# Optimization experiments

Measured on AMD Instinct MI355X. Metric: run time of the kernel, lower is better.

## Reference

```python
import jax, jax.numpy as jnp
import numpy as np

DIM = 2048
NUM_GATES = 8
TOP_N = 2
EPS = 1e-9
B, N = 2, 4096
CAPACITY_FACTOR = 1.25  # train
MIN_EXPERT_CAPACITY = 4
THRESHOLD = np.array([EPS, 0.2], dtype=np.float32)  # [eps, *threshold_train]


def setup_inputs() -> dict:
    key = jax.random.key(0)
    kx, kw, kp = jax.random.split(key, 3)
    x = jax.random.normal(kx, (B, N, DIM), jnp.float32)
    W = jax.random.normal(kw, (NUM_GATES, DIM), jnp.float32) * 0.02  # Linear(dim, num_gates, bias=False)
    probs = jax.random.uniform(kp, (TOP_N, B, N), jnp.float32)       # the uniform draw inside forward
    return {"x": x, "W": W, "probs": probs}


def reference(x, W, probs):
    b, n, d = x.shape
    cap = max(min(n, int(n * CAPACITY_FACTOR / NUM_GATES)), MIN_EXPERT_CAPACITY)
    dt = x.dtype

    gate_logits = jnp.einsum('bnd,ed->bne', x, W)            # [b,n,e]
    raw_gates = jax.nn.softmax(gate_logits, axis=-1)
    gates, gate_idx = jax.lax.top_k(raw_gates, TOP_N)        # [b,n,k]
    gates = jnp.moveaxis(gates, -1, 0)                       # [k,b,n]
    gate_idx = jnp.moveaxis(gate_idx, -1, 0)                 # [k,b,n]
    one_hot_e = jax.nn.one_hot(gate_idx, NUM_GATES, dtype=dt)  # [k,b,n,e]

    denom = jnp.clip(gates.sum(0, keepdims=True), EPS, None)
    gates = gates / denom                                    # renormalized top-n gates

    thr = jnp.clip(jnp.asarray(THRESHOLD, dt), EPS, None)[:, None, None]
    should_route = probs < gates / thr                       # [k,b,n]
    should_route = should_route.at[0].set(True)              # top-1 always routes
    mask = one_hot_e * should_route[..., None].astype(dt)    # [k,b,n,e]

    # exclusive cumsum over the sequence dim (position of each token in its expert queue)
    mask_cumsum = jnp.cumsum(mask, axis=2) - mask            # [k,b,n,e]

    combine = jnp.zeros((b, n, NUM_GATES, cap), dt)
    prev_expert_count = jnp.zeros((b, 1, NUM_GATES), dt)
    final_masks = []
    for k in range(TOP_N):  # tiny fixed loop over top-n slots
        pos = (mask_cumsum[k] + prev_expert_count) * mask[k]          # [b,n,e]
        mk = mask[k] * (pos < float(cap)).astype(dt)                  # drop over-capacity tokens
        prev_expert_count = prev_expert_count + mk.sum(axis=1, keepdims=True)
        pos_flat = pos.sum(axis=-1)                                   # [b,n]
        mflat = mk.sum(axis=-1)                                       # [b,n] in {0,1}
        pos_oh = jax.nn.one_hot(pos_flat.astype(jnp.int32), cap, dtype=dt)  # out-of-range -> zeros (safe_one_hot)
        # gates_k * mask_flat * one_hot_e * pos_one_hot; mflat^2 == mflat, one_hot_e*mflat == mk
        combine = combine + jnp.einsum('bn,bne,bnc->bnec', gates[k] * mflat, mk, pos_oh)
        final_masks.append(mk)

    dispatch = (combine != 0).astype(dt)
    # straight-through dispatch tensor
    dispatch = dispatch + combine - jax.lax.stop_gradient(combine)

    # training losses (mask[0] was mutated in-place in torch -> use final capacity-clipped top-1 mask)
    density_1 = final_masks[0].mean(axis=1)                  # [b,e]
    density_1_proxy = raw_gates.mean(axis=1)                 # [b,e]
    balance_loss = (density_1_proxy * density_1).mean() * float(NUM_GATES ** 2)
    router_z_loss = jnp.mean(jnp.square(jax.nn.logsumexp(gate_logits, axis=-1)))

    return dispatch, combine, balance_loss, router_z_loss
```

## Files before the change

kernel.cpp:

```cpp
#include <hip/hip_runtime.h>


#define DIMX 2048
#define NG   8
#define NB   2
#define NSEQ 4096
#define NTOK (NB*NSEQ)
#define CAPE 640
#define ROW  (NG*CAPE)
#define DCNT ((size_t)NTOK*ROW)

typedef float vfloat4 __attribute__((ext_vector_type(4)));

struct Ws {
  int   pk[NTOK];
  float g0[NTOK];
  float g1[NTOK];
  float z2[NTOK];
  int   pos0[NTOK];
  int   pos1[NTOK];
  float raws[(size_t)NTOK*NG];
  float proxy[16];
  float zpart[16];
  int   cnt0[16];
};

__global__ __launch_bounds__(512) void kgate(const float* __restrict__ x,
                                             const float* __restrict__ W,
                                             const float* __restrict__ probs,
                                             Ws* __restrict__ ws) {
  int tid = threadIdx.x;
  int wave = tid >> 6, lane = tid & 63;
  int token = blockIdx.x * 8 + wave;

  const float4* xp = (const float4*)(x + (size_t)token * DIMX);
  const float4* W4 = (const float4*)W;

  float acc[NG] = {0.f,0.f,0.f,0.f,0.f,0.f,0.f,0.f};
#pragma unroll
  for (int j = 0; j < 8; ++j) {
    float4 xj = xp[j * 64 + lane];
#pragma unroll
    for (int e = 0; e < NG; ++e) {
      float4 w = W4[e * 512 + j * 64 + lane];
      acc[e] = fmaf(xj.x, w.x, acc[e]);
      acc[e] = fmaf(xj.y, w.y, acc[e]);
      acc[e] = fmaf(xj.z, w.z, acc[e]);
      acc[e] = fmaf(xj.w, w.w, acc[e]);
    }
  }
#pragma unroll
  for (int e = 0; e < NG; ++e) {
#pragma unroll
    for (int off = 32; off > 0; off >>= 1) acc[e] += __shfl_xor(acc[e], off, 64);
  }

  float m = acc[0];
#pragma unroll
  for (int e = 1; e < NG; ++e) m = fmaxf(m, acc[e]);
  float ex[NG], s = 0.f;
#pragma unroll
  for (int e = 0; e < NG; ++e) { ex[e] = expf(acc[e] - m); s += ex[e]; }
  float raw[NG];
#pragma unroll
  for (int e = 0; e < NG; ++e) raw[e] = ex[e] / s;

  int e0i = 0; float g0v = raw[0];
#pragma unroll
  for (int e = 1; e < NG; ++e) if (raw[e] > g0v) { g0v = raw[e]; e0i = e; }
  int e1i = -1; float g1v = -1.f;
#pragma unroll
  for (int e = 0; e < NG; ++e) if (e != e0i && raw[e] > g1v) { g1v = raw[e]; e1i = e; }

  float denom = g0v + g1v;
  if (denom < 1e-9f) denom = 1e-9f;
  float g0n = g0v / denom, g1n = g1v / denom;

  float p1 = probs[NTOK + token];
  int rte = (p1 < (g1n / 0.2f)) ? 1 : 0;

  float lse = m + logf(s);

  if (lane < NG) ws->raws[(size_t)token * NG + lane] = raw[lane];
  if (lane == 0) {
    ws->pk[token] = e0i | (e1i << 4) | (rte << 8);
    ws->g0[token] = g0n;  ws->g1[token] = g1n;
    ws->z2[token] = lse * lse;
  }
}

__global__ __launch_bounds__(256) void kscan(Ws* __restrict__ ws) {
  __shared__ int   wtot[4];
  __shared__ float wsum[4];
  __shared__ float zsum[4];
  int be = blockIdx.x, b = be >> 3, e = be & 7;
  int t = threadIdx.x, wave = t >> 6, lane = t & 63;
  int base = b * NSEQ;

  int pk[16];
  {
    const int4* pp = (const int4*)(ws->pk + base + t * 16);
#pragma unroll
    for (int j = 0; j < 4; ++j) {
      int4 v = pp[j];
      pk[4*j] = v.x; pk[4*j+1] = v.y; pk[4*j+2] = v.z; pk[4*j+3] = v.w;
    }
  }

  float ps = 0.f;
#pragma unroll
  for (int i = 0; i < 16; ++i) ps += ws->raws[(size_t)(base + t * 16 + i) * NG + e];
#pragma unroll
  for (int off = 32; off > 0; off >>= 1) ps += __shfl_xor(ps, off, 64);
  if (lane == 0) wsum[wave] = ps;

  float zs = 0.f;
  if (t < 128) {
    float4 v = ((const float4*)ws->z2)[be * 128 + t];
    zs = v.x + v.y + v.z + v.w;
  }
#pragma unroll
  for (int off = 32; off > 0; off >>= 1) zs += __shfl_xor(zs, off, 64);
  if (lane == 0) zsum[wave] = zs;

  int cnt = 0;
#pragma unroll
  for (int i = 0; i < 16; ++i) cnt += ((pk[i] & 15) == e);
  int incl = cnt;
#pragma unroll
  for (int off = 1; off < 64; off <<= 1) { int v = __shfl_up(incl, off, 64); if (lane >= off) incl += v; }
  if (lane == 63) wtot[wave] = incl;
  __syncthreads();
  int woff = 0, tot = 0;
#pragma unroll
  for (int w = 0; w < 4; ++w) { int v = wtot[w]; tot += v; if (w < wave) woff += v; }
  int c0 = min(tot, CAPE);
  int p = woff + incl - cnt;
#pragma unroll
  for (int i = 0; i < 16; ++i) {
    if ((pk[i] & 15) == e) { ws->pos0[base + t * 16 + i] = (p < CAPE) ? p : -1; ++p; }
  }
  __syncthreads();

  cnt = 0;
#pragma unroll
  for (int i = 0; i < 16; ++i) cnt += ((((pk[i] >> 4) & 15) == e) && (pk[i] & 0x100));
  incl = cnt;
#pragma unroll
  for (int off = 1; off < 64; off <<= 1) { int v = __shfl_up(incl, off, 64); if (lane >= off) incl += v; }
  if (lane == 63) wtot[wave] = incl;
  __syncthreads();
  woff = 0;
#pragma unroll
  for (int w = 0; w < 4; ++w) { int v = wtot[w]; if (w < wave) woff += v; }
  p = woff + incl - cnt;
#pragma unroll
  for (int i = 0; i < 16; ++i) {
    if ((((pk[i] >> 4) & 15) == e)) {
      if (pk[i] & 0x100) { int q = p + c0; ws->pos1[base + t * 16 + i] = (q < CAPE) ? q : -1; ++p; }
      else               { ws->pos1[base + t * 16 + i] = -1; }
    }
  }

  if (t == 0) {
    ws->proxy[be] = wsum[0] + wsum[1] + wsum[2] + wsum[3];
    ws->zpart[be] = zsum[0] + zsum[1] + zsum[2] + zsum[3];
    ws->cnt0[be]  = c0;
  }
}

__global__ __launch_bounds__(256) void kout(const Ws* __restrict__ ws, float* __restrict__ out) {
  int t = threadIdx.x;

#pragma unroll
  for (int tk = 0; tk < 2; ++tk) {
    int token = blockIdx.x * 2 + tk;
    int pkv = ws->pk[token];
    int e0 = pkv & 15, e1 = (pkv >> 4) & 15;
    int p0 = ws->pos0[token], p1 = ws->pos1[token];
    float g0 = ws->g0[token], g1 = ws->g1[token];
    int o0 = (p0 >= 0) ? e0 * CAPE + p0 : -16;
    int o1 = (p1 >= 0) ? e1 * CAPE + p1 : -16;

    float* drow = out + (size_t)token * ROW;
    float* crow = out + DCNT + (size_t)token * ROW;

#pragma unroll
    for (int c = 0; c < 5; ++c) {
      int off = c * 1024 + t * 4;
      int r0 = o0 - off, r1 = o1 - off;
      vfloat4 dv, cv;
      dv.x = ((r0 == 0) | (r1 == 0)) ? 1.f : 0.f;
      dv.y = ((r0 == 1) | (r1 == 1)) ? 1.f : 0.f;
      dv.z = ((r0 == 2) | (r1 == 2)) ? 1.f : 0.f;
      dv.w = ((r0 == 3) | (r1 == 3)) ? 1.f : 0.f;
      cv.x = (r0 == 0) ? g0 : ((r1 == 0) ? g1 : 0.f);
      cv.y = (r0 == 1) ? g0 : ((r1 == 1) ? g1 : 0.f);
      cv.z = (r0 == 2) ? g0 : ((r1 == 2) ? g1 : 0.f);
      cv.w = (r0 == 3) ? g0 : ((r1 == 3) ? g1 : 0.f);
      __builtin_nontemporal_store(dv, (vfloat4*)(drow + off));
      __builtin_nontemporal_store(cv, (vfloat4*)(crow + off));
    }
  }

  if (blockIdx.x == 0 && t == 0) {
    float bal = 0.f, z = 0.f;
#pragma unroll
    for (int i = 0; i < 16; ++i) {
      bal += (ws->proxy[i] * (1.f / NSEQ)) * ((float)ws->cnt0[i] * (1.f / NSEQ));
      z   += ws->zpart[i];
    }
    out[2 * DCNT]     = bal * 4.f;
    out[2 * DCNT + 1] = z * (1.f / NTOK);
  }
}

extern "C" void kernel_launch(void* const* d_in, const int* in_sizes, int n_in,
                              void* d_out, int out_size, void* d_ws, size_t ws_size,
                              hipStream_t stream) {
  const float* x     = (const float*)d_in[0];
  const float* W     = (const float*)d_in[1];
  const float* probs = (const float*)d_in[2];
  float* out = (float*)d_out;
  Ws* ws = (Ws*)d_ws;

  kgate<<<NTOK / 8, 512, 0, stream>>>(x, W, probs, ws);
  kscan<<<16, 256, 0, stream>>>(ws);
  kout<<<NTOK / 2, 256, 0, stream>>>(ws, out);
}
```

Baseline: 97.02 us.

## Zero dispatch tensor inside gate kernel and scatter ones in output kernel

The gate kernel gains extra blocks, interleaved with the gating blocks, that write zeros over the whole dispatch tensor. The aim is to overlap that store traffic with the memory-bound gate matmul and its reads of x. The output kernel then writes only the combine tensor densely and sets at most two dispatch entries per token to 1.0 with scalar stores. Total bytes written stay the same, so any gain depends on better overlap and less work in the last kernel, while the extra blocks compete with the gate blocks for bandwidth.

Result: faster. 90.22 us (-7.0%).

```diff
diff --git a/kernel.cpp b/kernel.cpp
--- a/kernel.cpp
+++ b/kernel.cpp
@@ -25,13 +25,37 @@
   int   cnt0[16];
 };
 
-__global__ __launch_bounds__(512) void kgate(const float* __restrict__ x,
-                                             const float* __restrict__ W,
-                                             const float* __restrict__ probs,
-                                             Ws* __restrict__ ws) {
+__global__ __launch_bounds__(512) void kfat(const float* __restrict__ x,
+                                            const float* __restrict__ W,
+                                            const float* __restrict__ probs,
+                                            Ws* __restrict__ ws,
+                                            float* __restrict__ out) {
+  int bid = blockIdx.x;
   int tid = threadIdx.x;
+
+  int g;
+  if (bid < 2048) {
+    g = bid >> 1;
+    if (!(bid & 1)) {
+      vfloat4* o4 = (vfloat4*)out;
+      long base = (long)g * 5120 + tid;
+      vfloat4 z = {0.f, 0.f, 0.f, 0.f};
+#pragma unroll
+      for (int k = 0; k < 10; ++k) __builtin_nontemporal_store(z, o4 + base + k * 512);
+      return;
+    }
+  } else {
+    int zb = bid - 1024;
+    vfloat4* o4 = (vfloat4*)out;
+    long base = (long)zb * 5120 + tid;
+    vfloat4 z = {0.f, 0.f, 0.f, 0.f};
+#pragma unroll
+    for (int k = 0; k < 10; ++k) __builtin_nontemporal_store(z, o4 + base + k * 512);
+    return;
+  }
+
   int wave = tid >> 6, lane = tid & 63;
-  int token = blockIdx.x * 8 + wave;
+  int token = g * 8 + wave;
 
   const float4* xp = (const float4*)(x + (size_t)token * DIMX);
   const float4* W4 = (const float4*)W;
@@ -169,7 +193,7 @@
   }
 }
 
-__global__ __launch_bounds__(256) void kout(const Ws* __restrict__ ws, float* __restrict__ out) {
+__global__ __launch_bounds__(256) void kcomb(const Ws* __restrict__ ws, float* __restrict__ out) {
   int t = threadIdx.x;
 
 #pragma unroll
@@ -189,17 +213,17 @@
     for (int c = 0; c < 5; ++c) {
       int off = c * 1024 + t * 4;
       int r0 = o0 - off, r1 = o1 - off;
-      vfloat4 dv, cv;
-      dv.x = ((r0 == 0) | (r1 == 0)) ? 1.f : 0.f;
-      dv.y = ((r0 == 1) | (r1 == 1)) ? 1.f : 0.f;
-      dv.z = ((r0 == 2) | (r1 == 2)) ? 1.f : 0.f;
-      dv.w = ((r0 == 3) | (r1 == 3)) ? 1.f : 0.f;
+      vfloat4 cv;
       cv.x = (r0 == 0) ? g0 : ((r1 == 0) ? g1 : 0.f);
       cv.y = (r0 == 1) ? g0 : ((r1 == 1) ? g1 : 0.f);
       cv.z = (r0 == 2) ? g0 : ((r1 == 2) ? g1 : 0.f);
       cv.w = (r0 == 3) ? g0 : ((r1 == 3) ? g1 : 0.f);
-      __builtin_nontemporal_store(dv, (vfloat4*)(drow + off));
       __builtin_nontemporal_store(cv, (vfloat4*)(crow + off));
+    }
+
+    if (t == 0) {
+      if (o0 >= 0) drow[o0] = 1.f;
+      if (o1 >= 0) drow[o1] = 1.f;
     }
   }
 
@@ -224,7 +248,7 @@
   float* out = (float*)d_out;
   Ws* ws = (Ws*)d_ws;
 
-  kgate<<<NTOK / 8, 512, 0, stream>>>(x, W, probs, ws);
+  kfat<<<3072, 512, 0, stream>>>(x, W, probs, ws, out);
   kscan<<<16, 256, 0, stream>>>(ws);
-  kout<<<NTOK / 2, 256, 0, stream>>>(ws, out);
-}
+  kcomb<<<NTOK / 2, 256, 0, stream>>>(ws, out);
+}
```
